# Performance work log

Hardware: AMD Instinct MI355X
Metric: run time of the kernel (lower is better)

Reference implementation:

```python
import jax, jax.numpy as jnp
import numpy as np

B, N, C, H = 4, 1024, 768, 12
D = C // H  # head_dim = 64


def setup_inputs() -> dict:
    key = jax.random.key(0)
    ks = jax.random.split(key, 16)
    def lin(k, fan_in, fan_out):
        # torch Linear init: U(-1/sqrt(fan_in), 1/sqrt(fan_in)); stored as [in, out]
        bound = 1.0 / np.sqrt(fan_in)
        kw, kb = jax.random.split(k)
        W = jax.random.uniform(kw, (fan_in, fan_out), minval=-bound, maxval=bound, dtype=jnp.float32)
        b = jax.random.uniform(kb, (fan_out,), minval=-bound, maxval=bound, dtype=jnp.float32)
        return W, b
    Wq, bq = lin(ks[0], C, C)
    Wk, bk = lin(ks[1], C, C)
    Wv, bv = lin(ks[2], C, C)
    Wo, bo = lin(ks[3], C, C)
    Wd1, bd1 = lin(ks[4], 1, 16)
    Wd2, bd2 = lin(ks[5], 16, H)
    x = jax.random.normal(ks[6], (B, N, C), dtype=jnp.float32)
    coords = jax.random.uniform(ks[7], (B, N, 2), dtype=jnp.float32)
    return {"x": x, "coords": coords,
            "Wq": Wq, "bq": bq, "Wk": Wk, "bk": bk, "Wv": Wv, "bv": bv,
            "Wo": Wo, "bo": bo, "Wd1": Wd1, "bd1": bd1, "Wd2": Wd2, "bd2": bd2}


def reference(x, coords, Wq, bq, Wk, bk, Wv, bv, Wo, bo, Wd1, bd1, Wd2, bd2):
    scale = D ** (-0.5)
    # projections -> [B, H, N, D]
    def heads(t):
        return t.reshape(B, N, H, D).transpose(0, 2, 1, 3)
    q = heads(x @ Wq + bq)
    k = heads(x @ Wk + bk)
    v = heads(x @ Wv + bv)
    # content scores [B, H, N, N]
    content = jnp.einsum('bhid,bhjd->bhij', q, k) * scale
    # pairwise distances [B, N, N, 1]
    diff = coords[:, :, None, :] - coords[:, None, :, :]
    dist = jnp.sqrt(jnp.sum(diff * diff, axis=-1, keepdims=True) + 1e-6)
    # distance MLP: 1 -> 16 -> H, then permute to [B, H, N, N]
    hbias = jax.nn.relu(dist @ Wd1 + bd1)
    spatial = (hbias @ Wd2 + bd2).transpose(0, 3, 1, 2)
    attn = jax.nn.softmax(content + spatial, axis=-1)
    out = jnp.einsum('bhij,bhjd->bhid', attn, v)
    out = out.transpose(0, 2, 1, 3).reshape(B, N, C)
    out = out @ Wo + bo
    return out, attn
```

## Files before the change

kernel.cpp:

```cpp
#include <hip/hip_runtime.h>
#include <cstddef>
#include <cstdint>

#define Bc 4
#define Nc 1024
#define Cc 768
#define Hc 12
#define Dc 64
#define BHc 48
#define QKV_ELEMS ((size_t)Bc * Nc * Cc)

typedef __attribute__((ext_vector_type(4))) unsigned int u32x4;
typedef __attribute__((ext_vector_type(8))) short s16x8;
typedef __attribute__((ext_vector_type(4))) float fx4;
typedef __attribute__((ext_vector_type(2))) float fx2;

union Frag { u32x4 u; s16x8 s; unsigned short h[8]; };

__device__ inline unsigned short f2bf(float x) {
    union { float f; uint32_t u; } c; c.f = x;
    return (unsigned short)((c.u + 0x7FFFu + ((c.u >> 16) & 1u)) >> 16);
}
__device__ inline float bf2f(unsigned short b) {
    union { uint32_t u; float f; } c; c.u = ((uint32_t)b) << 16;
    return c.f;
}

__global__ __launch_bounds__(256) void prep_w_kernel(
    const float* __restrict__ Wq, const float* __restrict__ Wk,
    const float* __restrict__ Wv, const float* __restrict__ Wo,
    unsigned short* __restrict__ Thi, unsigned short* __restrict__ Tlo)
{
    __shared__ float scr[64 * 65];
    const int mat = blockIdx.z;
    const float* W = (mat == 0) ? Wq : (mat == 1) ? Wk : (mat == 2) ? Wv : Wo;
    const int k0 = blockIdx.y * 64, n0 = blockIdx.x * 64;
    const int tid = threadIdx.x;

    #pragma unroll
    for (int it = 0; it < 4; ++it) {
        const int lin = tid + it * 256;
        const int r = lin >> 4, c4 = (lin & 15) << 2;
        const fx4 v = *(const fx4*)&W[(size_t)(k0 + r) * 768 + n0 + c4];
        scr[r * 65 + c4 + 0] = v[0]; scr[r * 65 + c4 + 1] = v[1];
        scr[r * 65 + c4 + 2] = v[2]; scr[r * 65 + c4 + 3] = v[3];
    }
    __syncthreads();
    unsigned short* th = Thi + (size_t)mat * 768 * 768;
    unsigned short* tl = Tlo + (size_t)mat * 768 * 768;
    #pragma unroll
    for (int it = 0; it < 16; ++it) {
        const int lin = tid + it * 256;
        const int n = lin >> 6, kq = lin & 63;
        const float val = scr[kq * 65 + n];
        const size_t o = (size_t)(n0 + n) * 768 + k0 + kq;
        const unsigned short hb = f2bf(val);
        th[o] = hb;
        tl[o] = f2bf(val - bf2f(hb));
    }
}

__global__ __launch_bounds__(256) void prep_tables_kernel(
    const float* __restrict__ Wd1, const float* __restrict__ bd1,
    const float* __restrict__ Wd2, const float* __restrict__ bd2,
    float* __restrict__ knots, float* __restrict__ alphaT, float* __restrict__ betaT)
{
    __shared__ float w1s[16], b1s[16], kn[16];
    __shared__ int rank[16];
    const int tid = threadIdx.x;
    if (tid < 16) {
        const float w1 = Wd1[tid], b1 = bd1[tid];
        w1s[tid] = w1; b1s[tid] = b1;
        kn[tid] = (w1 != 0.0f) ? (-b1 / w1) : INFINITY;
    }
    __syncthreads();
    if (tid < 16) {
        int rk = 0;
        for (int u = 0; u < 16; ++u) {
            const float ku = kn[u], km = kn[tid];
            if (ku < km || (ku == km && u < tid)) ++rk;
        }
        rank[tid] = rk;
        knots[tid] = kn[tid];
    }
    __syncthreads();
    if (tid < 17 * 12) {
        const int s = tid / 12, h = tid % 12;
        float a = 0.0f, be = bd2[h];
        for (int u = 0; u < 16; ++u) {
            const float w1 = w1s[u], b1 = b1s[u];
            bool act;
            if (w1 > 0.0f)      act = (rank[u] < s);
            else if (w1 < 0.0f) act = (rank[u] >= s);
            else                act = (b1 > 0.0f);
            if (act) {
                const float w2 = Wd2[u * 12 + h];
                a  += w2 * w1;
                be += w2 * b1;
            }
        }
        alphaT[s * 12 + h] = a;
        betaT[s * 12 + h]  = be;
    }
}

struct SmemG { u32x4 ah[8 * 64]; u32x4 al[8 * 64]; u32x4 bh[8 * 64]; u32x4 bl[8 * 64]; };
struct SmemT { float scr[64 * 65]; };
union SmemU { SmemG g; SmemT t; };

template<int AMODE, int OMODE>
__global__ __launch_bounds__(256) void gemm_mfma_kernel(
    const float* __restrict__ Af,
    const unsigned short* __restrict__ Ahi, const unsigned short* __restrict__ Alo,
    const unsigned short* __restrict__ Bhi, const unsigned short* __restrict__ Blo,
    const float* __restrict__ bias,
    float* __restrict__ outF,
    unsigned short* __restrict__ Ohi, unsigned short* __restrict__ Olo)
{
    __shared__ SmemU sm;
    const int tid = threadIdx.x;
    const int w = tid >> 6, L = tid & 63;
    const int Lr = L & 15, Lg = L >> 4;
    const int m0 = blockIdx.y * 64, n0 = blockIdx.x * 64;

    fx4 acc[2][2] = {};

    for (int kk = 0; kk < 768; kk += 64) {
        if (AMODE == 0) {
            #pragma unroll
            for (int it = 0; it < 2; ++it) {
                const int slot = tid + it * 256;
                const int s = slot >> 6, l = slot & 63;
                const int row = m0 + ((s >> 1) << 4) + (l & 15);
                const int kb = kk + ((s & 1) << 5) + ((l >> 4) << 3);
                const fx4 v0 = *(const fx4*)&Af[(size_t)row * 768 + kb];
                const fx4 v1 = *(const fx4*)&Af[(size_t)row * 768 + kb + 4];
                float vv[8] = {v0[0], v0[1], v0[2], v0[3], v1[0], v1[1], v1[2], v1[3]};
                Frag fh, fl;
                #pragma unroll
                for (int e = 0; e < 8; ++e) {
                    const unsigned short hb = f2bf(vv[e]);
                    fh.h[e] = hb;
                    fl.h[e] = f2bf(vv[e] - bf2f(hb));
                }
                sm.g.ah[slot] = fh.u;
                sm.g.al[slot] = fl.u;
            }
        } else {
            #pragma unroll
            for (int it = 0; it < 2; ++it) {
                const int slot = tid + it * 256;
                const int s = slot >> 6, l = slot & 63;
                const int row = m0 + ((s >> 1) << 4) + (l & 15);
                const int kb = kk + ((s & 1) << 5) + ((l >> 4) << 3);
                sm.g.ah[slot] = *(const u32x4*)&Ahi[(size_t)row * 768 + kb];
                sm.g.al[slot] = *(const u32x4*)&Alo[(size_t)row * 768 + kb];
            }
        }
        #pragma unroll
        for (int it = 0; it < 2; ++it) {
            const int slot = tid + it * 256;
            const int s = slot >> 6, l = slot & 63;
            const int col = n0 + ((s >> 1) << 4) + (l & 15);
            const int kb = kk + ((s & 1) << 5) + ((l >> 4) << 3);
            sm.g.bh[slot] = *(const u32x4*)&Bhi[(size_t)col * 768 + kb];
            sm.g.bl[slot] = *(const u32x4*)&Blo[(size_t)col * 768 + kb];
        }
        __syncthreads();
        #pragma unroll
        for (int kc = 0; kc < 2; ++kc) {
            Frag ah[2], al[2], bh[2], bl[2];
            #pragma unroll
            for (int mm = 0; mm < 2; ++mm) {
                const int rg = (w >> 1) * 2 + mm;
                ah[mm].u = sm.g.ah[(rg * 2 + kc) * 64 + L];
                al[mm].u = sm.g.al[(rg * 2 + kc) * 64 + L];
            }
            #pragma unroll
            for (int nn = 0; nn < 2; ++nn) {
                const int cg = (w & 1) * 2 + nn;
                bh[nn].u = sm.g.bh[(cg * 2 + kc) * 64 + L];
                bl[nn].u = sm.g.bl[(cg * 2 + kc) * 64 + L];
            }
            #pragma unroll
            for (int mm = 0; mm < 2; ++mm)
                #pragma unroll
                for (int nn = 0; nn < 2; ++nn) {
                    acc[mm][nn] = __builtin_amdgcn_mfma_f32_16x16x32_bf16(ah[mm].s, bh[nn].s, acc[mm][nn], 0, 0, 0);
                    acc[mm][nn] = __builtin_amdgcn_mfma_f32_16x16x32_bf16(ah[mm].s, bl[nn].s, acc[mm][nn], 0, 0, 0);
                    acc[mm][nn] = __builtin_amdgcn_mfma_f32_16x16x32_bf16(al[mm].s, bh[nn].s, acc[mm][nn], 0, 0, 0);
                }
        }
        __syncthreads();
    }

    if (OMODE == 0 || OMODE == 2) {
        #pragma unroll
        for (int mm = 0; mm < 2; ++mm) {
            const int row = m0 + (w >> 1) * 32 + mm * 16 + Lg * 4;
            #pragma unroll
            for (int nn = 0; nn < 2; ++nn) {
                const int col = n0 + (w & 1) * 32 + nn * 16 + Lr;
                const float bs = bias[col];
                #pragma unroll
                for (int r = 0; r < 4; ++r) {
                    const float val = acc[mm][nn][r] + bs;
                    if (OMODE == 2) {
                        outF[(size_t)(row + r) * 768 + col] = val;
                    } else {
                        const int b = (row + r) >> 10, nloc = (row + r) & 1023;
                        const int h = col >> 6, d = col & 63;
                        const size_t o = (((size_t)(b * Hc + h) * Nc + nloc) << 6) + d;
                        const unsigned short hb = f2bf(val);
                        Ohi[o] = hb;
                        Olo[o] = f2bf(val - bf2f(hb));
                    }
                }
            }
        }
    } else {
        #pragma unroll
        for (int mm = 0; mm < 2; ++mm) {
            const int rl = (w >> 1) * 32 + mm * 16 + Lg * 4;
            #pragma unroll
            for (int nn = 0; nn < 2; ++nn) {
                const int cl = (w & 1) * 32 + nn * 16 + Lr;
                const float bs = bias[n0 + cl];
                #pragma unroll
                for (int r = 0; r < 4; ++r)
                    sm.t.scr[(rl + r) * 65 + cl] = acc[mm][nn][r] + bs;
            }
        }
        __syncthreads();
        const int b = m0 >> 10, h = n0 >> 6, nbase = m0 & 1023;
        #pragma unroll
        for (int it = 0; it < 16; ++it) {
            const int lin = tid + it * 256;
            const int dd = lin >> 6, j = lin & 63;
            const float val = sm.t.scr[j * 65 + dd];
            const size_t o = (size_t)((b * Hc + h) * Dc + dd) * Nc + nbase + j;
            const unsigned short hb = f2bf(val);
            Ohi[o] = hb;
            Olo[o] = f2bf(val - bf2f(hb));
        }
    }
}

__global__ __launch_bounds__(256) void scores_mfma_kernel(
    const unsigned short* __restrict__ qhi, const unsigned short* __restrict__ qlo,
    const unsigned short* __restrict__ khi, const unsigned short* __restrict__ klo,
    const float* __restrict__ coords,
    const float* __restrict__ knots_g, const float* __restrict__ alphaT,
    const float* __restrict__ betaT,
    float* __restrict__ attn, float* __restrict__ ml)
{
    __shared__ u32x4 KsH[8 * 64], KsL[8 * 64];
    __shared__ float cjx[64], cjy[64];
    __shared__ float aH[17], bH[17];

    const int tid = threadIdx.x;
    const int w = tid >> 6, L = tid & 63;
    const int Lr = L & 15, Lg = L >> 4;
    const int bh = blockIdx.y, b = bh / Hc, h = bh % Hc;
    const int i0 = blockIdx.x * 64;
    const int wrow = i0 + w * 16;

    if (tid < 17) { aH[tid] = alphaT[tid * 12 + h]; bH[tid] = betaT[tid * 12 + h]; }
    float kn[16];
    #pragma unroll
    for (int t = 0; t < 16; ++t) kn[t] = knots_g[t];

    Frag qh[2], ql[2];
    #pragma unroll
    for (int kc = 0; kc < 2; ++kc) {
        const size_t o = ((size_t)bh * Nc + wrow + Lr) * 64 + kc * 32 + Lg * 8;
        qh[kc].u = *(const u32x4*)&qhi[o];
        ql[kc].u = *(const u32x4*)&qlo[o];
    }
    float cix4[4], ciy4[4];
    #pragma unroll
    for (int r = 0; r < 4; ++r) {
        const fx2 cc = *(const fx2*)&coords[((size_t)b * Nc + wrow + Lg * 4 + r) * 2];
        cix4[r] = cc[0]; ciy4[r] = cc[1];
    }

    float m_r[4] = {-INFINITY, -INFINITY, -INFINITY, -INFINITY};
    float l_r[4] = {0.f, 0.f, 0.f, 0.f};

    for (int jt = 0; jt < 16; ++jt) {
        #pragma unroll
        for (int it = 0; it < 2; ++it) {
            const int slot = tid + it * 256;
            const int s = slot >> 6, l = slot & 63;
            const int jrow = jt * 64 + ((s >> 1) << 4) + (l & 15);
            const int kb = ((s & 1) << 5) + ((l >> 4) << 3);
            const size_t o = ((size_t)bh * Nc + jrow) * 64 + kb;
            KsH[slot] = *(const u32x4*)&khi[o];
            KsL[slot] = *(const u32x4*)&klo[o];
        }
        if (tid < 64) {
            const fx2 cc = *(const fx2*)&coords[((size_t)b * Nc + jt * 64 + tid) * 2];
            cjx[tid] = cc[0]; cjy[tid] = cc[1];
        }
        __syncthreads();

        fx4 acc[4] = {};
        #pragma unroll
        for (int kc = 0; kc < 2; ++kc) {
            #pragma unroll
            for (int cg = 0; cg < 4; ++cg) {
                Frag kbh, kbl;
                kbh.u = KsH[(cg * 2 + kc) * 64 + L];
                kbl.u = KsL[(cg * 2 + kc) * 64 + L];
                acc[cg] = __builtin_amdgcn_mfma_f32_16x16x32_bf16(qh[kc].s, kbh.s, acc[cg], 0, 0, 0);
                acc[cg] = __builtin_amdgcn_mfma_f32_16x16x32_bf16(qh[kc].s, kbl.s, acc[cg], 0, 0, 0);
                acc[cg] = __builtin_amdgcn_mfma_f32_16x16x32_bf16(ql[kc].s, kbh.s, acc[cg], 0, 0, 0);
            }
        }

        float sv[4][4];
        #pragma unroll
        for (int cg = 0; cg < 4; ++cg) {
            const int jl = cg * 16 + Lr;
            const float cx = cjx[jl], cy = cjy[jl];
            #pragma unroll
            for (int r = 0; r < 4; ++r) {
                const float dx = cix4[r] - cx, dy = ciy4[r] - cy;
                const float dist = sqrtf(fmaf(dx, dx, fmaf(dy, dy, 1e-6f)));
                int idx = 0;
                #pragma unroll
                for (int t = 0; t < 16; ++t) idx += (dist > kn[t]) ? 1 : 0;
                const float sp = fmaf(aH[idx], dist, bH[idx]);
                sv[cg][r] = fmaf(acc[cg][r], 0.125f, sp);
            }
        }
        #pragma unroll
        for (int r = 0; r < 4; ++r) {
            const int row = wrow + Lg * 4 + r;
            #pragma unroll
            for (int cg = 0; cg < 4; ++cg)
                attn[((size_t)bh * Nc + row) * Nc + jt * 64 + cg * 16 + Lr] = sv[cg][r];
        }
        #pragma unroll
        for (int r = 0; r < 4; ++r) {
            float tm = fmaxf(fmaxf(sv[0][r], sv[1][r]), fmaxf(sv[2][r], sv[3][r]));
            #pragma unroll
            for (int off = 1; off < 16; off <<= 1)
                tm = fmaxf(tm, __shfl_xor(tm, off));
            const float mnew = fmaxf(m_r[r], tm);
            float ts = __expf(sv[0][r] - mnew) + __expf(sv[1][r] - mnew)
                     + __expf(sv[2][r] - mnew) + __expf(sv[3][r] - mnew);
            #pragma unroll
            for (int off = 1; off < 16; off <<= 1)
                ts += __shfl_xor(ts, off);
            l_r[r] = l_r[r] * __expf(m_r[r] - mnew) + ts;
            m_r[r] = mnew;
        }
        __syncthreads();
    }

    if (Lr == 0) {
        #pragma unroll
        for (int r = 0; r < 4; ++r) {
            const size_t row = (size_t)bh * Nc + wrow + Lg * 4 + r;
            ml[row * 2 + 0] = m_r[r];
            ml[row * 2 + 1] = l_r[r];
        }
    }
}

__global__ __launch_bounds__(256) void pv_mfma_kernel(
    float* __restrict__ attn,
    const unsigned short* __restrict__ vThi, const unsigned short* __restrict__ vTlo,
    const float* __restrict__ ml,
    unsigned short* __restrict__ Hhi, unsigned short* __restrict__ Hlo)
{
    __shared__ u32x4 VsH[8 * 64], VsL[8 * 64];
    const int tid = threadIdx.x;
    const int w = tid >> 6, L = tid & 63;
    const int Lr = L & 15, Lg = L >> 4;
    const int bh = blockIdx.y, b = bh / Hc, h = bh % Hc;
    const int i0 = blockIdx.x * 64;
    const int wrow = i0 + w * 16;

    const size_t prow = (size_t)bh * Nc + wrow + Lr;
    const float mrow = ml[prow * 2 + 0];
    const float il = 1.0f / ml[prow * 2 + 1];

    fx4 acc[4] = {};

    for (int jt = 0; jt < 16; ++jt) {
        #pragma unroll
        for (int it = 0; it < 2; ++it) {
            const int slot = tid + it * 256;
            const int s = slot >> 6, l = slot & 63;
            const int dd = ((s >> 1) << 4) + (l & 15);
            const int jb = jt * 64 + ((s & 1) << 5) + ((l >> 4) << 3);
            const size_t o = ((size_t)bh * Dc + dd) * Nc + jb;
            VsH[slot] = *(const u32x4*)&vThi[o];
            VsL[slot] = *(const u32x4*)&vTlo[o];
        }
        __syncthreads();

        #pragma unroll
        for (int kc = 0; kc < 2; ++kc) {
            float* ap = &attn[prow * Nc + jt * 64 + kc * 32 + Lg * 8];
            const fx4 s0 = *(const fx4*)ap;
            const fx4 s1 = *(const fx4*)(ap + 4);
            float p[8];
            p[0] = __expf(s0[0] - mrow) * il; p[1] = __expf(s0[1] - mrow) * il;
            p[2] = __expf(s0[2] - mrow) * il; p[3] = __expf(s0[3] - mrow) * il;
            p[4] = __expf(s1[0] - mrow) * il; p[5] = __expf(s1[1] - mrow) * il;
            p[6] = __expf(s1[2] - mrow) * il; p[7] = __expf(s1[3] - mrow) * il;
            fx4 w0, w1;
            w0[0] = p[0]; w0[1] = p[1]; w0[2] = p[2]; w0[3] = p[3];
            w1[0] = p[4]; w1[1] = p[5]; w1[2] = p[6]; w1[3] = p[7];
            *(fx4*)ap = w0;
            *(fx4*)(ap + 4) = w1;
            Frag ph, pl;
            #pragma unroll
            for (int e = 0; e < 8; ++e) {
                const unsigned short hb = f2bf(p[e]);
                ph.h[e] = hb;
                pl.h[e] = f2bf(p[e] - bf2f(hb));
            }
            #pragma unroll
            for (int dg = 0; dg < 4; ++dg) {
                Frag vh, vl;
                vh.u = VsH[(dg * 2 + kc) * 64 + L];
                vl.u = VsL[(dg * 2 + kc) * 64 + L];
                acc[dg] = __builtin_amdgcn_mfma_f32_16x16x32_bf16(ph.s, vh.s, acc[dg], 0, 0, 0);
                acc[dg] = __builtin_amdgcn_mfma_f32_16x16x32_bf16(ph.s, vl.s, acc[dg], 0, 0, 0);
                acc[dg] = __builtin_amdgcn_mfma_f32_16x16x32_bf16(pl.s, vh.s, acc[dg], 0, 0, 0);
            }
        }
        __syncthreads();
    }

    #pragma unroll
    for (int dg = 0; dg < 4; ++dg) {
        #pragma unroll
        for (int r = 0; r < 4; ++r) {
            const int i = wrow + Lg * 4 + r;
            const int col = h * 64 + dg * 16 + Lr;
            const float val = acc[dg][r];
            const size_t o = (size_t)(b * Nc + i) * Cc + col;
            const unsigned short hb = f2bf(val);
            Hhi[o] = hb;
            Hlo[o] = f2bf(val - bf2f(hb));
        }
    }
}

extern "C" void kernel_launch(void* const* d_in, const int* in_sizes, int n_in,
                              void* d_out, int out_size, void* d_ws, size_t ws_size,
                              hipStream_t stream)
{
    (void)in_sizes; (void)n_in; (void)out_size; (void)ws_size;

    const float* x      = (const float*)d_in[0];
    const float* coords = (const float*)d_in[1];
    const float* Wq = (const float*)d_in[2];  const float* bq = (const float*)d_in[3];
    const float* Wk = (const float*)d_in[4];  const float* bk = (const float*)d_in[5];
    const float* Wv = (const float*)d_in[6];  const float* bv = (const float*)d_in[7];
    const float* Wo = (const float*)d_in[8];  const float* bo = (const float*)d_in[9];
    const float* Wd1 = (const float*)d_in[10]; const float* bd1 = (const float*)d_in[11];
    const float* Wd2 = (const float*)d_in[12]; const float* bd2 = (const float*)d_in[13];

    float* out_main = (float*)d_out;
    float* attn     = out_main + QKV_ELEMS;

    uint8_t* wsb = (uint8_t*)d_ws;
    const size_t SZ_BF = (size_t)BHc * Nc * Dc * 2;
    const size_t SZ_W  = (size_t)768 * 768 * 2;
    unsigned short* qhi  = (unsigned short*)(wsb + 0 * SZ_BF);
    unsigned short* qlo  = (unsigned short*)(wsb + 1 * SZ_BF);
    unsigned short* khi  = (unsigned short*)(wsb + 2 * SZ_BF);
    unsigned short* klo  = (unsigned short*)(wsb + 3 * SZ_BF);
    unsigned short* vThi = (unsigned short*)(wsb + 4 * SZ_BF);
    unsigned short* vTlo = (unsigned short*)(wsb + 5 * SZ_BF);
    unsigned short* Thi  = (unsigned short*)(wsb + 6 * SZ_BF);
    unsigned short* Tlo  = (unsigned short*)(wsb + 6 * SZ_BF + 4 * SZ_W);
    float* mlp    = (float*)(wsb + 6 * SZ_BF + 8 * SZ_W);
    float* knots  = mlp + (size_t)BHc * Nc * 2;
    float* alphaT = knots + 16;
    float* betaT  = alphaT + 17 * 12;

    prep_w_kernel<<<dim3(12, 12, 4), 256, 0, stream>>>(Wq, Wk, Wv, Wo, Thi, Tlo);
    prep_tables_kernel<<<1, 256, 0, stream>>>(Wd1, bd1, Wd2, bd2, knots, alphaT, betaT);

    dim3 gGemm(12, 64);
    gemm_mfma_kernel<0, 0><<<gGemm, 256, 0, stream>>>(
        x, nullptr, nullptr, Thi + 0 * 768 * 768, Tlo + 0 * 768 * 768, bq,
        nullptr, qhi, qlo);
    gemm_mfma_kernel<0, 0><<<gGemm, 256, 0, stream>>>(
        x, nullptr, nullptr, Thi + 1 * 768 * 768, Tlo + 1 * 768 * 768, bk,
        nullptr, khi, klo);
    gemm_mfma_kernel<0, 1><<<gGemm, 256, 0, stream>>>(
        x, nullptr, nullptr, Thi + 2 * 768 * 768, Tlo + 2 * 768 * 768, bv,
        nullptr, vThi, vTlo);

    scores_mfma_kernel<<<dim3(16, 48), 256, 0, stream>>>(
        qhi, qlo, khi, klo, coords, knots, alphaT, betaT, attn, mlp);

    pv_mfma_kernel<<<dim3(16, 48), 256, 0, stream>>>(
        attn, vThi, vTlo, mlp, qhi, qlo);

    gemm_mfma_kernel<1, 2><<<gGemm, 256, 0, stream>>>(
        nullptr, qhi, qlo, Thi + 3 * 768 * 768, Tlo + 3 * 768 * 768, bo,
        out_main, nullptr, nullptr);
}
```

Before: 403.4 us.

## Split attention over key halves, pre-split x, vectorize GEMM epilogues, prune knots

```diff
diff --git a/kernel.cpp b/kernel.cpp
--- a/kernel.cpp
+++ b/kernel.cpp
@@ -24,6 +24,16 @@
 __device__ inline float bf2f(unsigned short b) {
     union { uint32_t u; float f; } c; c.u = ((uint32_t)b) << 16;
     return c.f;
+}
+__device__ inline void split8(const float* v, u32x4& hi, u32x4& lo) {
+    Frag fh, fl;
+    #pragma unroll
+    for (int e = 0; e < 8; ++e) {
+        const unsigned short hb = f2bf(v[e]);
+        fh.h[e] = hb;
+        fl.h[e] = f2bf(v[e] - bf2f(hb));
+    }
+    hi = fh.u; lo = fl.u;
 }
 
 __global__ __launch_bounds__(256) void prep_w_kernel(
@@ -63,7 +73,7 @@
 __global__ __launch_bounds__(256) void prep_tables_kernel(
     const float* __restrict__ Wd1, const float* __restrict__ bd1,
     const float* __restrict__ Wd2, const float* __restrict__ bd2,
-    float* __restrict__ knots, float* __restrict__ alphaT, float* __restrict__ betaT)
+    float* __restrict__ abPack, float* __restrict__ kact, int* __restrict__ meta)
 {
     __shared__ float w1s[16], b1s[16], kn[16];
     __shared__ int rank[16];
@@ -81,7 +91,15 @@
             if (ku < km || (ku == km && u < tid)) ++rk;
         }
         rank[tid] = rk;
-        knots[tid] = kn[tid];
+    }
+    if (tid == 0) {
+        int nn = 0, na = 0;
+        for (int t = 0; t < 16; ++t) {
+            const float kt = kn[t];
+            if (kt < 0.00099f) ++nn;
+            else if (kt < 1.41422f) kact[na++] = kt;
+        }
+        meta[0] = nn; meta[1] = na;
     }
     __syncthreads();
     if (tid < 17 * 12) {
@@ -99,19 +117,34 @@
                 be += w2 * b1;
             }
         }
-        alphaT[s * 12 + h] = a;
-        betaT[s * 12 + h]  = be;
-    }
-}
-
-struct SmemG { u32x4 ah[8 * 64]; u32x4 al[8 * 64]; u32x4 bh[8 * 64]; u32x4 bl[8 * 64]; };
-struct SmemT { float scr[64 * 65]; };
+        abPack[tid * 2 + 0] = a;
+        abPack[tid * 2 + 1] = be;
+    }
+}
+
+__global__ __launch_bounds__(256) void split_x_kernel(
+    const float* __restrict__ x, unsigned short* __restrict__ xhi,
+    unsigned short* __restrict__ xlo)
+{
+    const size_t t = (size_t)blockIdx.x * 256 + threadIdx.x;
+    float vv[8];
+    const fx4 a = *(const fx4*)&x[t * 8];
+    const fx4 b = *(const fx4*)&x[t * 8 + 4];
+    vv[0]=a[0]; vv[1]=a[1]; vv[2]=a[2]; vv[3]=a[3];
+    vv[4]=b[0]; vv[5]=b[1]; vv[6]=b[2]; vv[7]=b[3];
+    u32x4 hi, lo; split8(vv, hi, lo);
+    *(u32x4*)&xhi[t * 8] = hi;
+    *(u32x4*)&xlo[t * 8] = lo;
+}
+
+struct SmemG { u32x4 ah[512]; u32x4 al[512]; u32x4 bh[512]; u32x4 bl[512]; };
+struct SmemT { float scr[64 * 68]; };
 union SmemU { SmemG g; SmemT t; };
 
 template<int AMODE, int OMODE>
 __global__ __launch_bounds__(256) void gemm_mfma_kernel(
-    const float* __restrict__ Af,
     const unsigned short* __restrict__ Ahi, const unsigned short* __restrict__ Alo,
+    const float* __restrict__ P0, const float* __restrict__ P1,
     const unsigned short* __restrict__ Bhi, const unsigned short* __restrict__ Blo,
     const float* __restrict__ bias,
     float* __restrict__ outF,
@@ -126,43 +159,28 @@
     fx4 acc[2][2] = {};
 
     for (int kk = 0; kk < 768; kk += 64) {
-        if (AMODE == 0) {
-            #pragma unroll
-            for (int it = 0; it < 2; ++it) {
-                const int slot = tid + it * 256;
-                const int s = slot >> 6, l = slot & 63;
-                const int row = m0 + ((s >> 1) << 4) + (l & 15);
-                const int kb = kk + ((s & 1) << 5) + ((l >> 4) << 3);
-                const fx4 v0 = *(const fx4*)&Af[(size_t)row * 768 + kb];
-                const fx4 v1 = *(const fx4*)&Af[(size_t)row * 768 + kb + 4];
-                float vv[8] = {v0[0], v0[1], v0[2], v0[3], v1[0], v1[1], v1[2], v1[3]};
-                Frag fh, fl;
-                #pragma unroll
-                for (int e = 0; e < 8; ++e) {
-                    const unsigned short hb = f2bf(vv[e]);
-                    fh.h[e] = hb;
-                    fl.h[e] = f2bf(vv[e] - bf2f(hb));
-                }
-                sm.g.ah[slot] = fh.u;
-                sm.g.al[slot] = fl.u;
-            }
-        } else {
-            #pragma unroll
-            for (int it = 0; it < 2; ++it) {
-                const int slot = tid + it * 256;
-                const int s = slot >> 6, l = slot & 63;
-                const int row = m0 + ((s >> 1) << 4) + (l & 15);
-                const int kb = kk + ((s & 1) << 5) + ((l >> 4) << 3);
-                sm.g.ah[slot] = *(const u32x4*)&Ahi[(size_t)row * 768 + kb];
-                sm.g.al[slot] = *(const u32x4*)&Alo[(size_t)row * 768 + kb];
-            }
-        }
         #pragma unroll
         for (int it = 0; it < 2; ++it) {
             const int slot = tid + it * 256;
             const int s = slot >> 6, l = slot & 63;
-            const int col = n0 + ((s >> 1) << 4) + (l & 15);
+            const int row = m0 + ((s >> 1) << 4) + (l & 15);
             const int kb = kk + ((s & 1) << 5) + ((l >> 4) << 3);
+            if (AMODE == 1) {
+                sm.g.ah[slot] = *(const u32x4*)&Ahi[(size_t)row * 768 + kb];
+                sm.g.al[slot] = *(const u32x4*)&Alo[(size_t)row * 768 + kb];
+            } else {
+                const fx4 a0 = *(const fx4*)&P0[(size_t)row * 768 + kb];
+                const fx4 a1 = *(const fx4*)&P0[(size_t)row * 768 + kb + 4];
+                const fx4 c0 = *(const fx4*)&P1[(size_t)row * 768 + kb];
+                const fx4 c1 = *(const fx4*)&P1[(size_t)row * 768 + kb + 4];
+                float vv[8];
+                vv[0]=a0[0]+c0[0]; vv[1]=a0[1]+c0[1]; vv[2]=a0[2]+c0[2]; vv[3]=a0[3]+c0[3];
+                vv[4]=a1[0]+c1[0]; vv[5]=a1[1]+c1[1]; vv[6]=a1[2]+c1[2]; vv[7]=a1[3]+c1[3];
+                u32x4 hi, lo; split8(vv, hi, lo);
+                sm.g.ah[slot] = hi;
+                sm.g.al[slot] = lo;
+            }
+            const int col = n0 + ((s >> 1) << 4) + (l & 63 & 15);
             sm.g.bh[slot] = *(const u32x4*)&Bhi[(size_t)col * 768 + kb];
             sm.g.bl[slot] = *(const u32x4*)&Blo[(size_t)col * 768 + kb];
         }
@@ -194,114 +212,113 @@
         __syncthreads();
     }
 
-    if (OMODE == 0 || OMODE == 2) {
-        #pragma unroll
-        for (int mm = 0; mm < 2; ++mm) {
-            const int row = m0 + (w >> 1) * 32 + mm * 16 + Lg * 4;
-            #pragma unroll
-            for (int nn = 0; nn < 2; ++nn) {
-                const int col = n0 + (w & 1) * 32 + nn * 16 + Lr;
-                const float bs = bias[col];
-                #pragma unroll
-                for (int r = 0; r < 4; ++r) {
-                    const float val = acc[mm][nn][r] + bs;
-                    if (OMODE == 2) {
-                        outF[(size_t)(row + r) * 768 + col] = val;
-                    } else {
-                        const int b = (row + r) >> 10, nloc = (row + r) & 1023;
-                        const int h = col >> 6, d = col & 63;
-                        const size_t o = (((size_t)(b * Hc + h) * Nc + nloc) << 6) + d;
-                        const unsigned short hb = f2bf(val);
-                        Ohi[o] = hb;
-                        Olo[o] = f2bf(val - bf2f(hb));
-                    }
-                }
-            }
+    #pragma unroll
+    for (int mm = 0; mm < 2; ++mm) {
+        const int rl = (w >> 1) * 32 + mm * 16 + Lg * 4;
+        #pragma unroll
+        for (int nn = 0; nn < 2; ++nn) {
+            const int cl = (w & 1) * 32 + nn * 16 + Lr;
+            const float bs = bias[n0 + cl];
+            #pragma unroll
+            for (int r = 0; r < 4; ++r)
+                sm.t.scr[(rl + r) * 68 + cl] = acc[mm][nn][r] + bs;
+        }
+    }
+    __syncthreads();
+
+    if (OMODE == 0) {
+        const int h = n0 >> 6;
+        #pragma unroll
+        for (int it = 0; it < 2; ++it) {
+            const int t = tid + it * 256;
+            const int r = t >> 3, d0 = (t & 7) << 3;
+            float vv[8];
+            #pragma unroll
+            for (int e = 0; e < 8; ++e) vv[e] = sm.t.scr[r * 68 + d0 + e];
+            u32x4 hi, lo; split8(vv, hi, lo);
+            const int rg = m0 + r, b = rg >> 10, nloc = rg & 1023;
+            const size_t o = (((size_t)(b * Hc + h) * Nc + nloc) << 6) + d0;
+            *(u32x4*)&Ohi[o] = hi;
+            *(u32x4*)&Olo[o] = lo;
+        }
+    } else if (OMODE == 1) {
+        const int b = m0 >> 10, h = n0 >> 6, nbase = m0 & 1023;
+        #pragma unroll
+        for (int it = 0; it < 2; ++it) {
+            const int t = tid + it * 256;
+            const int dd = t >> 3, j0 = (t & 7) << 3;
+            float vv[8];
+            #pragma unroll
+            for (int e = 0; e < 8; ++e) vv[e] = sm.t.scr[(j0 + e) * 68 + dd];
+            u32x4 hi, lo; split8(vv, hi, lo);
+            const size_t o = (size_t)((b * Hc + h) * Dc + dd) * Nc + nbase + j0;
+            *(u32x4*)&Ohi[o] = hi;
+            *(u32x4*)&Olo[o] = lo;
         }
     } else {
         #pragma unroll
-        for (int mm = 0; mm < 2; ++mm) {
-            const int rl = (w >> 1) * 32 + mm * 16 + Lg * 4;
-            #pragma unroll
-            for (int nn = 0; nn < 2; ++nn) {
-                const int cl = (w & 1) * 32 + nn * 16 + Lr;
-                const float bs = bias[n0 + cl];
-                #pragma unroll
-                for (int r = 0; r < 4; ++r)
-                    sm.t.scr[(rl + r) * 65 + cl] = acc[mm][nn][r] + bs;
-            }
-        }
-        __syncthreads();
-        const int b = m0 >> 10, h = n0 >> 6, nbase = m0 & 1023;
-        #pragma unroll
-        for (int it = 0; it < 16; ++it) {
+        for (int it = 0; it < 4; ++it) {
             const int lin = tid + it * 256;
-            const int dd = lin >> 6, j = lin & 63;
-            const float val = sm.t.scr[j * 65 + dd];
-            const size_t o = (size_t)((b * Hc + h) * Dc + dd) * Nc + nbase + j;
-            const unsigned short hb = f2bf(val);
-            Ohi[o] = hb;
-            Olo[o] = f2bf(val - bf2f(hb));
-        }
-    }
-}
-
-__global__ __launch_bounds__(256) void scores_mfma_kernel(
+            const int r = lin >> 4, c4 = (lin & 15) << 2;
+            const fx4 v = *(const fx4*)&sm.t.scr[r * 68 + c4];
+            *(fx4*)&outF[(size_t)(m0 + r) * 768 + n0 + c4] = v;
+        }
+    }
+}
+
+__global__ __launch_bounds__(256, 4) void scores_half_kernel(
     const unsigned short* __restrict__ qhi, const unsigned short* __restrict__ qlo,
     const unsigned short* __restrict__ khi, const unsigned short* __restrict__ klo,
     const float* __restrict__ coords,
-    const float* __restrict__ knots_g, const float* __restrict__ alphaT,
-    const float* __restrict__ betaT,
+    const float* __restrict__ abPack, const float* __restrict__ kact,
+    const int* __restrict__ meta,
     float* __restrict__ attn, float* __restrict__ ml)
 {
-    __shared__ u32x4 KsH[8 * 64], KsL[8 * 64];
-    __shared__ float cjx[64], cjy[64];
-    __shared__ float aH[17], bH[17];
+    __shared__ u32x4 KsH[512], KsL[512];
+    __shared__ fx2 cjs[512];
+    __shared__ fx2 abt[17];
+    __shared__ float kacts[16];
+    __shared__ int metas[2];
 
     const int tid = threadIdx.x;
     const int w = tid >> 6, L = tid & 63;
     const int Lr = L & 15, Lg = L >> 4;
-    const int bh = blockIdx.y, b = bh / Hc, h = bh % Hc;
-    const int i0 = blockIdx.x * 64;
-    const int wrow = i0 + w * 16;
-
-    if (tid < 17) { aH[tid] = alphaT[tid * 12 + h]; bH[tid] = betaT[tid * 12 + h]; }
-    float kn[16];
-    #pragma unroll
-    for (int t = 0; t < 16; ++t) kn[t] = knots_g[t];
+    const int bh = blockIdx.z, b = bh / Hc, h = bh % Hc;
+    const int i0 = blockIdx.x * 64, half = blockIdx.y;
+    const int i = i0 + w * 16 + Lr;
+    const int Lg4 = Lg * 4;
+
+    if (tid < 17) abt[tid] = *(const fx2*)&abPack[(tid * Hc + h) * 2];
+    else if (tid >= 32 && tid < 48) kacts[tid - 32] = kact[tid - 32];
+    else if (tid == 64) { metas[0] = meta[0]; metas[1] = meta[1]; }
+    for (int t = tid; t < 512; t += 256)
+        cjs[t] = *(const fx2*)&coords[((size_t)b * Nc + half * 512 + t) * 2];
 
     Frag qh[2], ql[2];
     #pragma unroll
     for (int kc = 0; kc < 2; ++kc) {
-        const size_t o = ((size_t)bh * Nc + wrow + Lr) * 64 + kc * 32 + Lg * 8;
+        const size_t o = ((size_t)bh * Nc + i) * 64 + kc * 32 + Lg * 8;
         qh[kc].u = *(const u32x4*)&qhi[o];
         ql[kc].u = *(const u32x4*)&qlo[o];
     }
-    float cix4[4], ciy4[4];
-    #pragma unroll
-    for (int r = 0; r < 4; ++r) {
-        const fx2 cc = *(const fx2*)&coords[((size_t)b * Nc + wrow + Lg * 4 + r) * 2];
-        cix4[r] = cc[0]; ciy4[r] = cc[1];
-    }
-
-    float m_r[4] = {-INFINITY, -INFINITY, -INFINITY, -INFINITY};
-    float l_r[4] = {0.f, 0.f, 0.f, 0.f};
-
-    for (int jt = 0; jt < 16; ++jt) {
+    const fx2 ci = *(const fx2*)&coords[((size_t)b * Nc + i) * 2];
+    __syncthreads();
+    const int n_neg = metas[0], n_act = metas[1];
+
+    float m_r = -INFINITY, l_r = 0.f;
+    const size_t rowbase = ((size_t)bh * Nc + i) * Nc + half * 512;
+
+    for (int jt = 0; jt < 8; ++jt) {
         #pragma unroll
         for (int it = 0; it < 2; ++it) {
             const int slot = tid + it * 256;
             const int s = slot >> 6, l = slot & 63;
-            const int jrow = jt * 64 + ((s >> 1) << 4) + (l & 15);
+            const int jrow = half * 512 + jt * 64 + ((s >> 1) << 4) + (l & 15);
             const int kb = ((s & 1) << 5) + ((l >> 4) << 3);
             const size_t o = ((size_t)bh * Nc + jrow) * 64 + kb;
             KsH[slot] = *(const u32x4*)&khi[o];
             KsL[slot] = *(const u32x4*)&klo[o];
         }
-        if (tid < 64) {
-            const fx2 cc = *(const fx2*)&coords[((size_t)b * Nc + jt * 64 + tid) * 2];
-            cjx[tid] = cc[0]; cjy[tid] = cc[1];
-        }
         __syncthreads();
 
         fx4 acc[4] = {};
@@ -309,94 +326,99 @@
         for (int kc = 0; kc < 2; ++kc) {
             #pragma unroll
             for (int cg = 0; cg < 4; ++cg) {
-                Frag kbh, kbl;
-                kbh.u = KsH[(cg * 2 + kc) * 64 + L];
-                kbl.u = KsL[(cg * 2 + kc) * 64 + L];
-                acc[cg] = __builtin_amdgcn_mfma_f32_16x16x32_bf16(qh[kc].s, kbh.s, acc[cg], 0, 0, 0);
-                acc[cg] = __builtin_amdgcn_mfma_f32_16x16x32_bf16(qh[kc].s, kbl.s, acc[cg], 0, 0, 0);
-                acc[cg] = __builtin_amdgcn_mfma_f32_16x16x32_bf16(ql[kc].s, kbh.s, acc[cg], 0, 0, 0);
-            }
-        }
-
-        float sv[4][4];
+                Frag kh_, kl_;
+                kh_.u = KsH[(cg * 2 + kc) * 64 + L];
+                kl_.u = KsL[(cg * 2 + kc) * 64 + L];
+                acc[cg] = __builtin_amdgcn_mfma_f32_16x16x32_bf16(kh_.s, qh[kc].s, acc[cg], 0, 0, 0);
+                acc[cg] = __builtin_amdgcn_mfma_f32_16x16x32_bf16(kl_.s, qh[kc].s, acc[cg], 0, 0, 0);
+                acc[cg] = __builtin_amdgcn_mfma_f32_16x16x32_bf16(kh_.s, ql[kc].s, acc[cg], 0, 0, 0);
+            }
+        }
+
+        float sv[16];
         #pragma unroll
         for (int cg = 0; cg < 4; ++cg) {
-            const int jl = cg * 16 + Lr;
-            const float cx = cjx[jl], cy = cjy[jl];
+            float dist4[4]; int idx4[4];
             #pragma unroll
             for (int r = 0; r < 4; ++r) {
-                const float dx = cix4[r] - cx, dy = ciy4[r] - cy;
-                const float dist = sqrtf(fmaf(dx, dx, fmaf(dy, dy, 1e-6f)));
-                int idx = 0;
+                const fx2 cj = cjs[jt * 64 + cg * 16 + Lg4 + r];
+                const float dx = ci[0] - cj[0], dy = ci[1] - cj[1];
+                dist4[r] = sqrtf(fmaf(dx, dx, fmaf(dy, dy, 1e-6f)));
+                idx4[r] = n_neg;
+            }
+            for (int t = 0; t < n_act; ++t) {
+                const float kt = kacts[t];
                 #pragma unroll
-                for (int t = 0; t < 16; ++t) idx += (dist > kn[t]) ? 1 : 0;
-                const float sp = fmaf(aH[idx], dist, bH[idx]);
-                sv[cg][r] = fmaf(acc[cg][r], 0.125f, sp);
-            }
-        }
-        #pragma unroll
-        for (int r = 0; r < 4; ++r) {
-            const int row = wrow + Lg * 4 + r;
-            #pragma unroll
-            for (int cg = 0; cg < 4; ++cg)
-                attn[((size_t)bh * Nc + row) * Nc + jt * 64 + cg * 16 + Lr] = sv[cg][r];
-        }
-        #pragma unroll
-        for (int r = 0; r < 4; ++r) {
-            float tm = fmaxf(fmaxf(sv[0][r], sv[1][r]), fmaxf(sv[2][r], sv[3][r]));
-            #pragma unroll
-            for (int off = 1; off < 16; off <<= 1)
-                tm = fmaxf(tm, __shfl_xor(tm, off));
-            const float mnew = fmaxf(m_r[r], tm);
-            float ts = __expf(sv[0][r] - mnew) + __expf(sv[1][r] - mnew)
-                     + __expf(sv[2][r] - mnew) + __expf(sv[3][r] - mnew);
-            #pragma unroll
-            for (int off = 1; off < 16; off <<= 1)
-                ts += __shfl_xor(ts, off);
-            l_r[r] = l_r[r] * __expf(m_r[r] - mnew) + ts;
-            m_r[r] = mnew;
-        }
+                for (int r = 0; r < 4; ++r) idx4[r] += (dist4[r] > kt) ? 1 : 0;
+            }
+            #pragma unroll
+            for (int r = 0; r < 4; ++r) {
+                const fx2 ab = abt[idx4[r]];
+                sv[cg * 4 + r] = fmaf(acc[cg][r], 0.125f, fmaf(ab[0], dist4[r], ab[1]));
+            }
+        }
+
+        #pragma unroll
+        for (int cg = 0; cg < 4; ++cg) {
+            fx4 st;
+            st[0] = sv[cg*4+0]; st[1] = sv[cg*4+1]; st[2] = sv[cg*4+2]; st[3] = sv[cg*4+3];
+            *(fx4*)&attn[rowbase + jt * 64 + cg * 16 + Lg4] = st;
+        }
+
+        float tm = sv[0];
+        #pragma unroll
+        for (int e = 1; e < 16; ++e) tm = fmaxf(tm, sv[e]);
+        tm = fmaxf(tm, __shfl_xor(tm, 16));
+        tm = fmaxf(tm, __shfl_xor(tm, 32));
+        const float mnew = fmaxf(m_r, tm);
+        float ts = 0.f;
+        #pragma unroll
+        for (int e = 0; e < 16; ++e) ts += __expf(sv[e] - mnew);
+        ts += __shfl_xor(ts, 16);
+        ts += __shfl_xor(ts, 32);
+        l_r = l_r * __expf(m_r - mnew) + ts;
+        m_r = mnew;
         __syncthreads();
     }
 
-    if (Lr == 0) {
-        #pragma unroll
-        for (int r = 0; r < 4; ++r) {
-            const size_t row = (size_t)bh * Nc + wrow + Lg * 4 + r;
-            ml[row * 2 + 0] = m_r[r];
-            ml[row * 2 + 1] = l_r[r];
-        }
-    }
-}
-
-__global__ __launch_bounds__(256) void pv_mfma_kernel(
+    if (Lg == 0) {
+        const size_t mo = (((size_t)bh * Nc + i) * 2 + half) * 2;
+        ml[mo + 0] = m_r;
+        ml[mo + 1] = l_r;
+    }
+}
+
+__global__ __launch_bounds__(256, 4) void pv_half_kernel(
     float* __restrict__ attn,
     const unsigned short* __restrict__ vThi, const unsigned short* __restrict__ vTlo,
     const float* __restrict__ ml,
-    unsigned short* __restrict__ Hhi, unsigned short* __restrict__ Hlo)
-{
-    __shared__ u32x4 VsH[8 * 64], VsL[8 * 64];
+    float* __restrict__ Hp)
+{
+    __shared__ u32x4 VsH[512], VsL[512];
     const int tid = threadIdx.x;
     const int w = tid >> 6, L = tid & 63;
     const int Lr = L & 15, Lg = L >> 4;
-    const int bh = blockIdx.y, b = bh / Hc, h = bh % Hc;
-    const int i0 = blockIdx.x * 64;
+    const int bh = blockIdx.z, b = bh / Hc, h = bh % Hc;
+    const int i0 = blockIdx.x * 64, half = blockIdx.y;
     const int wrow = i0 + w * 16;
 
     const size_t prow = (size_t)bh * Nc + wrow + Lr;
-    const float mrow = ml[prow * 2 + 0];
-    const float il = 1.0f / ml[prow * 2 + 1];
+    const fx4 m4 = *(const fx4*)&ml[prow * 4];
+    const float mm = fmaxf(m4[0], m4[2]);
+    const float ll = m4[1] * __expf(m4[0] - mm) + m4[3] * __expf(m4[2] - mm);
+    const float il = 1.0f / ll;
 
     fx4 acc[4] = {};
 
-    for (int jt = 0; jt < 16; ++jt) {
+    for (int jt = 0; jt < 8; ++jt) {
+        const int jglob = half * 8 + jt;
         #pragma unroll
         for (int it = 0; it < 2; ++it) {
             const int slot = tid + it * 256;
             const int s = slot >> 6, l = slot & 63;
             const int dd = ((s >> 1) << 4) + (l & 15);
-            const int jb = jt * 64 + ((s & 1) << 5) + ((l >> 4) << 3);
-            const size_t o = ((size_t)bh * Dc + dd) * Nc + jb;
+            const int j = jglob * 64 + ((s & 1) << 5) + ((l >> 4) << 3);
+            const size_t o = ((size_t)bh * Dc + dd) * Nc + j;
             VsH[slot] = *(const u32x4*)&vThi[o];
             VsL[slot] = *(const u32x4*)&vTlo[o];
         }
@@ -404,26 +426,21 @@
 
         #pragma unroll
         for (int kc = 0; kc < 2; ++kc) {
-            float* ap = &attn[prow * Nc + jt * 64 + kc * 32 + Lg * 8];
+            float* ap = &attn[prow * Nc + jglob * 64 + kc * 32 + Lg * 8];
             const fx4 s0 = *(const fx4*)ap;
             const fx4 s1 = *(const fx4*)(ap + 4);
             float p[8];
-            p[0] = __expf(s0[0] - mrow) * il; p[1] = __expf(s0[1] - mrow) * il;
-            p[2] = __expf(s0[2] - mrow) * il; p[3] = __expf(s0[3] - mrow) * il;
-            p[4] = __expf(s1[0] - mrow) * il; p[5] = __expf(s1[1] - mrow) * il;
-            p[6] = __expf(s1[2] - mrow) * il; p[7] = __expf(s1[3] - mrow) * il;
+            p[0] = __expf(s0[0] - mm) * il; p[1] = __expf(s0[1] - mm) * il;
+            p[2] = __expf(s0[2] - mm) * il; p[3] = __expf(s0[3] - mm) * il;
+            p[4] = __expf(s1[0] - mm) * il; p[5] = __expf(s1[1] - mm) * il;
+            p[6] = __expf(s1[2] - mm) * il; p[7] = __expf(s1[3] - mm) * il;
             fx4 w0, w1;
-            w0[0] = p[0]; w0[1] = p[1]; w0[2] = p[2]; w0[3] = p[3];
-            w1[0] = p[4]; w1[1] = p[5]; w1[2] = p[6]; w1[3] = p[7];
+            w0[0]=p[0]; w0[1]=p[1]; w0[2]=p[2]; w0[3]=p[3];
+            w1[0]=p[4]; w1[1]=p[5]; w1[2]=p[6]; w1[3]=p[7];
             *(fx4*)ap = w0;
             *(fx4*)(ap + 4) = w1;
-            Frag ph, pl;
-            #pragma unroll
-            for (int e = 0; e < 8; ++e) {
-                const unsigned short hb = f2bf(p[e]);
-                ph.h[e] = hb;
-                pl.h[e] = f2bf(p[e] - bf2f(hb));
-            }
+            u32x4 phi, plo; split8(p, phi, plo);
+            Frag ph, pl; ph.u = phi; pl.u = plo;
             #pragma unroll
             for (int dg = 0; dg < 4; ++dg) {
                 Frag vh, vl;
@@ -438,18 +455,13 @@
     }
 
     #pragma unroll
-    for (int dg = 0; dg < 4; ++dg) {
+    for (int dg = 0; dg < 4; ++dg)
         #pragma unroll
         for (int r = 0; r < 4; ++r) {
-            const int i = wrow + Lg * 4 + r;
-            const int col = h * 64 + dg * 16 + Lr;
-            const float val = acc[dg][r];
-            const size_t o = (size_t)(b * Nc + i) * Cc + col;
-            const unsigned short hb = f2bf(val);
-            Hhi[o] = hb;
-            Hlo[o] = f2bf(val - bf2f(hb));
-        }
-    }
+            const int irow = wrow + Lg * 4 + r;
+            Hp[(size_t)half * QKV_ELEMS + ((size_t)b * Nc + irow) * Cc + h * Dc + dg * 16 + Lr]
+                = acc[dg][r];
+        }
 }
 
 extern "C" void kernel_launch(void* const* d_in, const int* in_sizes, int n_in,
@@ -472,41 +484,45 @@
 
     uint8_t* wsb = (uint8_t*)d_ws;
     const size_t SZ_BF = (size_t)BHc * Nc * Dc * 2;
-    const size_t SZ_W  = (size_t)768 * 768 * 2;
+    const size_t SZ_W4 = (size_t)4 * 768 * 768 * 2;
     unsigned short* qhi  = (unsigned short*)(wsb + 0 * SZ_BF);
     unsigned short* qlo  = (unsigned short*)(wsb + 1 * SZ_BF);
     unsigned short* khi  = (unsigned short*)(wsb + 2 * SZ_BF);
     unsigned short* klo  = (unsigned short*)(wsb + 3 * SZ_BF);
     unsigned short* vThi = (unsigned short*)(wsb + 4 * SZ_BF);
     unsigned short* vTlo = (unsigned short*)(wsb + 5 * SZ_BF);
-    unsigned short* Thi  = (unsigned short*)(wsb + 6 * SZ_BF);
-    unsigned short* Tlo  = (unsigned short*)(wsb + 6 * SZ_BF + 4 * SZ_W);
-    float* mlp    = (float*)(wsb + 6 * SZ_BF + 8 * SZ_W);
-    float* knots  = mlp + (size_t)BHc * Nc * 2;
-    float* alphaT = knots + 16;
-    float* betaT  = alphaT + 17 * 12;
+    float*          Hp   = (float*)(wsb + 0 * SZ_BF);
+    unsigned short* xhi  = (unsigned short*)(wsb + 6 * SZ_BF);
+    unsigned short* xlo  = (unsigned short*)(wsb + 7 * SZ_BF);
+    unsigned short* Thi  = (unsigned short*)(wsb + 8 * SZ_BF);
+    unsigned short* Tlo  = (unsigned short*)(wsb + 8 * SZ_BF + SZ_W4);
+    float* mlbuf  = (float*)(wsb + 8 * SZ_BF + 2 * SZ_W4);
+    float* abPack = mlbuf + (size_t)BHc * Nc * 4;
+    float* kact   = abPack + 17 * 12 * 2;
+    int*   meta   = (int*)(kact + 16);
 
     prep_w_kernel<<<dim3(12, 12, 4), 256, 0, stream>>>(Wq, Wk, Wv, Wo, Thi, Tlo);
-    prep_tables_kernel<<<1, 256, 0, stream>>>(Wd1, bd1, Wd2, bd2, knots, alphaT, betaT);
+    prep_tables_kernel<<<1, 256, 0, stream>>>(Wd1, bd1, Wd2, bd2, abPack, kact, meta);
+    split_x_kernel<<<dim3(1536), 256, 0, stream>>>(x, xhi, xlo);
 
     dim3 gGemm(12, 64);
-    gemm_mfma_kernel<0, 0><<<gGemm, 256, 0, stream>>>(
-        x, nullptr, nullptr, Thi + 0 * 768 * 768, Tlo + 0 * 768 * 768, bq,
-        nullptr, qhi, qlo);
-    gemm_mfma_kernel<0, 0><<<gGemm, 256, 0, stream>>>(
-        x, nullptr, nullptr, Thi + 1 * 768 * 768, Tlo + 1 * 768 * 768, bk,
-        nullptr, khi, klo);
-    gemm_mfma_kernel<0, 1><<<gGemm, 256, 0, stream>>>(
-        x, nullptr, nullptr, Thi + 2 * 768 * 768, Tlo + 2 * 768 * 768, bv,
-        nullptr, vThi, vTlo);
-
-    scores_mfma_kernel<<<dim3(16, 48), 256, 0, stream>>>(
-        qhi, qlo, khi, klo, coords, knots, alphaT, betaT, attn, mlp);
-
-    pv_mfma_kernel<<<dim3(16, 48), 256, 0, stream>>>(
-        attn, vThi, vTlo, mlp, qhi, qlo);
-
-    gemm_mfma_kernel<1, 2><<<gGemm, 256, 0, stream>>>(
-        nullptr, qhi, qlo, Thi + 3 * 768 * 768, Tlo + 3 * 768 * 768, bo,
-        out_main, nullptr, nullptr);
-}
+    gemm_mfma_kernel<1, 0><<<gGemm, 256, 0, stream>>>(
+        xhi, xlo, nullptr, nullptr, Thi + (size_t)0 * 768 * 768, Tlo + (size_t)0 * 768 * 768,
+        bq, nullptr, qhi, qlo);
+    gemm_mfma_kernel<1, 0><<<gGemm, 256, 0, stream>>>(
+        xhi, xlo, nullptr, nullptr, Thi + (size_t)1 * 768 * 768, Tlo + (size_t)1 * 768 * 768,
+        bk, nullptr, khi, klo);
+    gemm_mfma_kernel<1, 1><<<gGemm, 256, 0, stream>>>(
+        xhi, xlo, nullptr, nullptr, Thi + (size_t)2 * 768 * 768, Tlo + (size_t)2 * 768 * 768,
+        bv, nullptr, vThi, vTlo);
+
+    scores_half_kernel<<<dim3(16, 2, 48), 256, 0, stream>>>(
+        qhi, qlo, khi, klo, coords, abPack, kact, meta, attn, mlbuf);
+
+    pv_half_kernel<<<dim3(16, 2, 48), 256, 0, stream>>>(
+        attn, vThi, vTlo, mlbuf, Hp);
+
+    gemm_mfma_kernel<2, 2><<<gGemm, 256, 0, stream>>>(
+        nullptr, nullptr, Hp, Hp + QKV_ELEMS, Thi + (size_t)3 * 768 * 768,
+        Tlo + (size_t)3 * 768 * 768, bo, out_main, nullptr, nullptr);
+}
```

After: 404.6 us. About the same (+0.3%).
